# Kernel optimization log

Hardware: AMD Instinct MI355X
Metric: run time of the kernel (lower is better)

## Reference

```python
import jax, jax.numpy as jnp
import numpy as np
from jax import lax
from jax.scipy.linalg import lu_factor, lu_solve

NFEAT = 1024
NHID = 256   # QP variable dimension n
NCLS = 10
NEQ = 64     # equality constraints
QPEN = 0.1   # Qpenalty: Q = QPEN * I
ITERS = 12   # fixed Mehrotra predictor-corrector iterations
BATCH = 128


def setup_inputs() -> dict:
    key = jax.random.key(0)
    ks = jax.random.split(key, 6)
    x = jax.random.normal(ks[0], (BATCH, NFEAT), jnp.float32)
    W1 = jax.random.normal(ks[1], (NHID, NFEAT), jnp.float32) / np.sqrt(NFEAT)
    b1 = jnp.zeros((NHID,), jnp.float32)
    W2 = jax.random.normal(ks[2], (NCLS, NHID), jnp.float32) / np.sqrt(NHID)
    b2 = jnp.zeros((NCLS,), jnp.float32)
    A = jax.random.uniform(ks[3], (NEQ, NHID), jnp.float32)  # torch.rand in module
    return {"x": x, "W1": W1, "b1": b1, "W2": W2, "b2": b2, "A": A}


def _qp_solve(p, A):
    """Batched primal-dual interior-point solve of
        min_z 0.5*QPEN*||z||^2 + p.z   s.t.  A z = b (=1),  z >= 0
    which is the module's QP with Q=QPEN*I, G=-I, h=0, b=1.
    p: (B, n), A: (neq, n). Returns z: (B, n)."""
    B, n = p.shape
    neq = A.shape[0]
    N = n + neq
    b_eq = jnp.ones((neq,), p.dtype)
    rr = jnp.arange(n)

    # warm start: equality-constrained QP (ignore z>=0): [Q A'; A 0][z;nu]=[-p;b]
    K0 = jnp.zeros((N, N), p.dtype)
    K0 = K0.at[rr, rr].set(QPEN)
    K0 = K0.at[:n, n:].set(A.T).at[n:, :n].set(A)
    rhs0 = jnp.concatenate([-p, jnp.broadcast_to(b_eq, (B, neq))], axis=-1)
    sol0 = jnp.linalg.solve(K0, rhs0[..., None])[..., 0]
    z0 = sol0[:, :n]
    nu0 = sol0[:, n:]
    s0 = jnp.maximum(z0, 1.0)          # slack for -z + s = 0, kept positive
    lam0 = jnp.ones((B, n), p.dtype)   # ineq duals

    def step_len(v, dv, w, dw):
        def rat(a, da):
            safe = jnp.where(da < 0, da, -1.0)
            return jnp.where(da < 0, -a / safe, 1e10)
        m = jnp.min(jnp.minimum(rat(v, dv), rat(w, dw)), axis=-1)
        return jnp.minimum(1.0, 0.999 * m)  # (B,)

    def body(carry, _):
        z, s, lam, nu = carry
        rx = QPEN * z + p - lam + nu @ A      # Q z + p + G'lam + A'nu  (G=-I)
        ri = s - z                            # G z + s - h
        re = z @ A.T - b_eq                   # A z - b
        D = lam / s
        Hd = QPEN + D                         # (B, n) diag of Q + G'DG

        # reduced KKT: [[diag(Hd), A'],[A, 0]]  per sample
        K = jnp.zeros((B, N, N), p.dtype)
        K = K.at[:, rr, rr].set(Hd)
        K = K.at[:, :n, n:].set(A.T)
        K = K.at[:, n:, :n].set(A)
        lu, piv = lu_factor(K)

        def solve(rs):
            top = -rx + (lam * ri - rs) / s
            rhs = jnp.concatenate([top, -re], axis=-1)
            sol = lu_solve((lu, piv), rhs[..., None])[..., 0]
            dz = sol[:, :n]
            dnu = sol[:, n:]
            ds = dz - ri                      # ds = -ri - G dz
            dlam = (lam * ri - rs) / s - D * dz
            return dz, ds, dlam, dnu

        # predictor (affine)
        dz_a, ds_a, dlam_a, dnu_a = solve(lam * s)
        a_aff = step_len(s, ds_a, lam, dlam_a)[:, None]
        mu = jnp.mean(s * lam, axis=-1)
        mu_a = jnp.mean((s + a_aff * ds_a) * (lam + a_aff * dlam_a), axis=-1)
        sigma = (mu_a / mu) ** 3
        # corrector
        rs_c = lam * s + ds_a * dlam_a - (sigma * mu)[:, None]
        dz, ds, dlam, dnu = solve(rs_c)
        a = step_len(s, ds, lam, dlam)[:, None]
        z = z + a * dz
        nu = nu + a * dnu
        s = jnp.maximum(s + a * ds, 1e-8)
        lam = jnp.maximum(lam + a * dlam, 1e-8)
        return (z, s, lam, nu), None

    (z, _, _, _), _ = lax.scan(body, (z0, s0, lam0, nu0), None, length=ITERS)
    return z


def reference(x, W1, b1, W2, b2, A):
    h = jax.nn.relu(x @ W1.T + b1)            # fc1 + relu
    z = _qp_solve(-h, A)                      # QPFunction with p = -h
    logits = z @ W2.T + b2                    # fc2
    return jax.nn.log_softmax(logits, axis=-1)
```

## Files before the change

### kernel.cpp

```cpp
#include <hip/hip_runtime.h>
#include <math.h>

#define NTH 512

__device__ __forceinline__ float rl(float v, int ln) {
  return __int_as_float(__builtin_amdgcn_readlane(__float_as_int(v), ln));
}

__device__ __forceinline__ float dot64_row(const float4* __restrict__ As4,
                                           const float4* __restrict__ v4, int t) {
  float acc = 0.f;
#pragma unroll
  for (int q = 0; q < 16; ++q) {
    int qq = (q + t) & 15;
    float4 a = As4[t * 16 + qq];
    float4 b = v4[qq];
    acc = fmaf(a.x, b.x, acc); acc = fmaf(a.y, b.y, acc);
    acc = fmaf(a.z, b.z, acc); acc = fmaf(a.w, b.w, acc);
  }
  return acc;
}

__device__ __forceinline__ void fs_half(const float4* __restrict__ As4,
                                        const float4* __restrict__ wv4,
                                        int bi, int bj, int c0,
                                        float4& o0, float4& o1, float4& o2, float4& o3) {
  float a00=0,a01=0,a02=0,a03=0,a10=0,a11=0,a12=0,a13=0;
  float a20=0,a21=0,a22=0,a23=0,a30=0,a31=0,a32=0,a33=0;
  const int c40 = c0 >> 2;
  for (int c4 = c40; c4 < c40 + 32; ++c4) {
    float4 w4 = wv4[c4];
#pragma unroll
    for (int e = 0; e < 4; ++e) {
      float wc = (e==0)?w4.x:(e==1)?w4.y:(e==2)?w4.z:w4.w;
      int c = 4*c4 + e;
      float4 a4 = As4[c*16 + bi];
      float4 b4 = As4[c*16 + bj];
      float bx = b4.x*wc, by = b4.y*wc, bz = b4.z*wc, bw = b4.w*wc;
      a00=fmaf(a4.x,bx,a00); a01=fmaf(a4.x,by,a01); a02=fmaf(a4.x,bz,a02); a03=fmaf(a4.x,bw,a03);
      a10=fmaf(a4.y,bx,a10); a11=fmaf(a4.y,by,a11); a12=fmaf(a4.y,bz,a12); a13=fmaf(a4.y,bw,a13);
      a20=fmaf(a4.z,bx,a20); a21=fmaf(a4.z,by,a21); a22=fmaf(a4.z,bz,a22); a23=fmaf(a4.z,bw,a23);
      a30=fmaf(a4.w,bx,a30); a31=fmaf(a4.w,by,a31); a32=fmaf(a4.w,bz,a32); a33=fmaf(a4.w,bw,a33);
    }
  }
  o0 = make_float4(a00,a01,a02,a03);
  o1 = make_float4(a10,a11,a12,a13);
  o2 = make_float4(a20,a21,a22,a23);
  o3 = make_float4(a30,a31,a32,a33);
}

#define PSTEP8(VE, V1,V2,V3,V4,V5,V6,V7, LNE) {                        \
    float piv = __shfl(VE, (LNE), 64);                                 \
    float inv = 1.0f / piv;                                            \
    VE = (lane == (LNE)) ? inv : VE * inv;                             \
    float c1 = __shfl(V1,(LNE),64); V1 = (lane==(LNE))?(-c1*inv):fmaf(-c1,VE,V1); \
    float c2 = __shfl(V2,(LNE),64); V2 = (lane==(LNE))?(-c2*inv):fmaf(-c2,VE,V2); \
    float c3 = __shfl(V3,(LNE),64); V3 = (lane==(LNE))?(-c3*inv):fmaf(-c3,VE,V3); \
    float c4_ = __shfl(V4,(LNE),64); V4 = (lane==(LNE))?(-c4_*inv):fmaf(-c4_,VE,V4); \
    float c5 = __shfl(V5,(LNE),64); V5 = (lane==(LNE))?(-c5*inv):fmaf(-c5,VE,V5); \
    float c6 = __shfl(V6,(LNE),64); V6 = (lane==(LNE))?(-c6*inv):fmaf(-c6,VE,V6); \
    float c7 = __shfl(V7,(LNE),64); V7 = (lane==(LNE))?(-c7*inv):fmaf(-c7,VE,V7); \
  }

__device__ __forceinline__ void gj8(float* __restrict__ Sb, float* __restrict__ T,
                                    float* __restrict__ colb, int t) {
  float4* Sb4 = (float4*)Sb;
  float4* T4 = (float4*)T;
  float4* colb4 = (float4*)colb;
  const int lane = t & 63, wav = t >> 6;
  for (int p = 0; p < 8; ++p) {
    if (wav == 0) {
      float v0 = Sb[(8*p+0)*68 + lane];
      float v1 = Sb[(8*p+1)*68 + lane];
      float v2 = Sb[(8*p+2)*68 + lane];
      float v3 = Sb[(8*p+3)*68 + lane];
      float v4 = Sb[(8*p+4)*68 + lane];
      float v5 = Sb[(8*p+5)*68 + lane];
      float v6 = Sb[(8*p+6)*68 + lane];
      float v7 = Sb[(8*p+7)*68 + lane];
      PSTEP8(v0, v1,v2,v3,v4,v5,v6,v7, 8*p+0);
      PSTEP8(v1, v0,v2,v3,v4,v5,v6,v7, 8*p+1);
      PSTEP8(v2, v0,v1,v3,v4,v5,v6,v7, 8*p+2);
      PSTEP8(v3, v0,v1,v2,v4,v5,v6,v7, 8*p+3);
      PSTEP8(v4, v0,v1,v2,v3,v5,v6,v7, 8*p+4);
      PSTEP8(v5, v0,v1,v2,v3,v4,v6,v7, 8*p+5);
      PSTEP8(v6, v0,v1,v2,v3,v4,v5,v7, 8*p+6);
      PSTEP8(v7, v0,v1,v2,v3,v4,v5,v6, 8*p+7);
      T[0*64+lane]=v0; T[1*64+lane]=v1; T[2*64+lane]=v2; T[3*64+lane]=v3;
      T[4*64+lane]=v4; T[5*64+lane]=v5; T[6*64+lane]=v6; T[7*64+lane]=v7;
    } else if (wav == 1) {
      colb4[lane]      = *(const float4*)&Sb[lane*68 + 8*p];
      colb4[64 + lane] = *(const float4*)&Sb[lane*68 + 8*p + 4];
    }
    __syncthreads();
    float4 cA = colb4[lane];
    float4 cB = colb4[64 + lane];
    const bool rowsJ = ((lane >> 3) == p);
    const int e = lane & 7;
#pragma unroll
    for (int q = 0; q < 2; ++q) {
      const int c = 2*wav + q;
      if (rowsJ) {
        Sb4[lane*17 + c] = T4[e*16 + c];
      } else {
        float4 t0=T4[0*16+c], t1=T4[1*16+c], t2=T4[2*16+c], t3=T4[3*16+c];
        float4 t4=T4[4*16+c], t5=T4[5*16+c], t6=T4[6*16+c], t7=T4[7*16+c];
        float4 mv;
        if (c == 2*p || c == 2*p+1) { mv = make_float4(0.f,0.f,0.f,0.f); }
        else mv = Sb4[lane*17 + c];
        mv.x -= cA.x*t0.x + cA.y*t1.x + cA.z*t2.x + cA.w*t3.x
              + cB.x*t4.x + cB.y*t5.x + cB.z*t6.x + cB.w*t7.x;
        mv.y -= cA.x*t0.y + cA.y*t1.y + cA.z*t2.y + cA.w*t3.y
              + cB.x*t4.y + cB.y*t5.y + cB.z*t6.y + cB.w*t7.y;
        mv.z -= cA.x*t0.z + cA.y*t1.z + cA.z*t2.z + cA.w*t3.z
              + cB.x*t4.z + cB.y*t5.z + cB.z*t6.z + cB.w*t7.z;
        mv.w -= cA.x*t0.w + cA.y*t1.w + cA.z*t2.w + cA.w*t3.w
              + cB.x*t4.w + cB.y*t5.w + cB.z*t6.w + cB.w*t7.w;
        Sb4[lane*17 + c] = mv;
      }
    }
    __syncthreads();
  }
}

__device__ __forceinline__ float matS_lds(const float* __restrict__ Sb, float rh, int t) {
  const float4* Sb4 = (const float4*)Sb;
  float acc = 0.f;
#pragma unroll
  for (int m = 0; m < 16; ++m) {
    float4 s4 = Sb4[t*17 + m];
    acc = fmaf(s4.x, rl(rh, 4*m+0), acc);
    acc = fmaf(s4.y, rl(rh, 4*m+1), acc);
    acc = fmaf(s4.z, rl(rh, 4*m+2), acc);
    acc = fmaf(s4.w, rl(rh, 4*m+3), acc);
  }
  return acc;
}

__global__ __launch_bounds__(NTH, 1)
void optnet_kernel(const float* __restrict__ x,  const float* __restrict__ W1,
                   const float* __restrict__ b1, const float* __restrict__ W2,
                   const float* __restrict__ b2, const float* __restrict__ A,
                   float* __restrict__ out)
{
  extern __shared__ float sm[];
  const int b = blockIdx.x;
  const int t = threadIdx.x;
  const int lane = t & 63;
  const int wav = t >> 6;
  const bool owner = (t < 256);

  float* As    = sm;
  float* Sb    = sm + 16384;
  float* xld   = Sb;
  float* Pbuf  = sm + 20736;
  float* T     = Pbuf + 2176;
  float* colb  = T + 512;
  float* h     = colb + 512;
  float* z     = h + 256;
  float* wHd   = z + 256;
  float* wtp   = wHd + 256;
  float* partA = wtp + 256;
  float* partB = partA + 192;
  float* partB2= partB + 192;
  float* nu    = partB2 + 512;
  float* rev   = nu + 64;
  float* dnu   = rev + 64;
  float* red   = dnu + 64;

  const float4* As4  = (const float4*)As;
  float4*       Sb4  = (float4*)Sb;
  const float4* wv4  = (const float4*)wHd;
  const float4* nu4  = (const float4*)nu;
  const float4* dnu4 = (const float4*)dnu;
  float4*       Pb4  = (float4*)Pbuf;

  int bi = 0, bj = 0;
  if (t < 272) {
    int rr = (t < 136) ? t : (t - 136);
    while (rr >= 16 - bi) { rr -= 16 - bi; ++bi; }
    bj = bi + rr;
  }
  const int pg  = (t - 272) >> 6;
  const int plo = pg * 85 + (pg > 0 ? 1 : 0);
  const int phi = plo + 85 + (pg == 0 ? 1 : 0);

  for (int g = t; g < 64 * 256; g += NTH)
    As[(g & 255) * 64 + (g >> 8)] = A[g];
  for (int g = t; g < 1024; g += NTH)
    xld[g] = x[b * 1024 + g];
  __syncthreads();

  {
    const float4* xr = (const float4*)xld;
    for (int jj = 0; jj < 32; ++jj) {
      int j = (wav << 5) + jj;
      const float4* w1r = (const float4*)(W1 + (size_t)j * 1024);
      float acc = 0.f;
#pragma unroll
      for (int mm = 0; mm < 4; ++mm) {
        float4 a = w1r[lane + (mm << 6)];
        float4 xv = xr[lane + (mm << 6)];
        acc = fmaf(a.x,xv.x,fmaf(a.y,xv.y,fmaf(a.z,xv.z,fmaf(a.w,xv.w,acc))));
      }
#pragma unroll
      for (int off = 32; off > 0; off >>= 1) acc += __shfl_xor(acc, off, 64);
      if (lane == 0) { float v = acc + b1[j]; h[j] = v > 0.f ? v : 0.f; }
    }
  }
  __syncthreads();
  const float hr = h[t & 255];

  if (owner) { wHd[t] = 10.0f; wtp[t] = hr * 10.0f; }
  __syncthreads();
  float4 o0, o1, o2, o3;
  if (t < 272) {
    fs_half(As4, wv4, bi, bj, (t < 136) ? 0 : 128, o0, o1, o2, o3);
    if (t >= 136) {
      int tt = t - 136;
      Pb4[tt*4+0]=o0; Pb4[tt*4+1]=o1; Pb4[tt*4+2]=o2; Pb4[tt*4+3]=o3;
    }
  } else if (t < 464) {
    float accB = 0.f;
    for (int c = plo; c < phi; ++c)
      accB = fmaf(wtp[c], As[c * 64 + lane], accB);
    partB[pg * 64 + lane] = accB;
  }
  __syncthreads();
  if (t < 136) {
    float4 p0=Pb4[t*4+0], p1=Pb4[t*4+1], p2=Pb4[t*4+2], p3=Pb4[t*4+3];
    o0.x+=p0.x; o0.y+=p0.y; o0.z+=p0.z; o0.w+=p0.w;
    o1.x+=p1.x; o1.y+=p1.y; o1.z+=p1.z; o1.w+=p1.w;
    o2.x+=p2.x; o2.y+=p2.y; o2.z+=p2.z; o2.w+=p2.w;
    o3.x+=p3.x; o3.y+=p3.y; o3.z+=p3.z; o3.w+=p3.w;
    Sb4[(4*bi+0)*17 + bj] = o0;
    Sb4[(4*bi+1)*17 + bj] = o1;
    Sb4[(4*bi+2)*17 + bj] = o2;
    Sb4[(4*bi+3)*17 + bj] = o3;
    if (bi != bj) {
      Sb4[(4*bj+0)*17 + bi] = make_float4(o0.x,o1.x,o2.x,o3.x);
      Sb4[(4*bj+1)*17 + bi] = make_float4(o0.y,o1.y,o2.y,o3.y);
      Sb4[(4*bj+2)*17 + bi] = make_float4(o0.z,o1.z,o2.z,o3.z);
      Sb4[(4*bj+3)*17 + bi] = make_float4(o0.w,o1.w,o2.w,o3.w);
    }
  }
  __syncthreads();
  gj8(Sb, T, colb, t);
  if (t < 64) {
    float rh = partB[t] + partB[64 + t] + partB[128 + t] - 1.0f;
    nu[t] = matS_lds(Sb, rh, t);
  }
  __syncthreads();

  float zt = 0.f, st = 0.f, lt = 0.f;
  if (owner) {
    float atd = dot64_row(As4, nu4, t);
    zt = (hr - atd) * 10.0f;
    z[t] = zt;
    st = fmaxf(zt, 1.0f);
    lt = 1.0f;
  }
  __syncthreads();

  float rit = 0.f, Dt = 0.f, wt = 0.f, g1 = 0.f, top1 = 0.f, rxt = 0.f;
  for (int it = 0; it < 12; ++it) {
    if (owner) {
      const float nuA = dot64_row(As4, nu4, t);
      rxt = 0.1f * zt - hr - lt + nuA;
      rit = st - zt;
      Dt  = lt / st;
      wt  = 1.0f / (0.1f + Dt);
      const float rs1 = lt * st;
      g1  = (lt * rit - rs1) / st;
      top1 = -rxt + g1;
      wHd[t] = wt;
      wtp[t] = top1 * wt;
    }
    __syncthreads();
    if (t < 272) {
      fs_half(As4, wv4, bi, bj, (t < 136) ? 0 : 128, o0, o1, o2, o3);
      if (t >= 136) {
        int tt = t - 136;
        Pb4[tt*4+0]=o0; Pb4[tt*4+1]=o1; Pb4[tt*4+2]=o2; Pb4[tt*4+3]=o3;
      }
    } else if (t < 464) {
      float accA = 0.f, accB = 0.f;
      for (int c = plo; c < phi; ++c) {
        float av = As[c * 64 + lane];
        accA = fmaf(z[c],   av, accA);
        accB = fmaf(wtp[c], av, accB);
      }
      partA[pg * 64 + lane] = accA;
      partB[pg * 64 + lane] = accB;
    }
    __syncthreads();
    if (t < 136) {
      float4 p0=Pb4[t*4+0], p1=Pb4[t*4+1], p2=Pb4[t*4+2], p3=Pb4[t*4+3];
      o0.x+=p0.x; o0.y+=p0.y; o0.z+=p0.z; o0.w+=p0.w;
      o1.x+=p1.x; o1.y+=p1.y; o1.z+=p1.z; o1.w+=p1.w;
      o2.x+=p2.x; o2.y+=p2.y; o2.z+=p2.z; o2.w+=p2.w;
      o3.x+=p3.x; o3.y+=p3.y; o3.z+=p3.z; o3.w+=p3.w;
      Sb4[(4*bi+0)*17 + bj] = o0;
      Sb4[(4*bi+1)*17 + bj] = o1;
      Sb4[(4*bi+2)*17 + bj] = o2;
      Sb4[(4*bi+3)*17 + bj] = o3;
      if (bi != bj) {
        Sb4[(4*bj+0)*17 + bi] = make_float4(o0.x,o1.x,o2.x,o3.x);
        Sb4[(4*bj+1)*17 + bi] = make_float4(o0.y,o1.y,o2.y,o3.y);
        Sb4[(4*bj+2)*17 + bi] = make_float4(o0.z,o1.z,o2.z,o3.z);
        Sb4[(4*bj+3)*17 + bi] = make_float4(o0.w,o1.w,o2.w,o3.w);
      }
    }
    __syncthreads();
    gj8(Sb, T, colb, t);
    if (t < 64) {
      float re_t = partA[t] + partA[64 + t] + partA[128 + t] - 1.0f;
      rev[t] = re_t;
      float rh = partB[t] + partB[64 + t] + partB[128 + t] + re_t;
      dnu[t] = matS_lds(Sb, rh, t);
    }
    __syncthreads();
    float dsa = 0.f, dla = 0.f;
    if (owner) {
      float atd = dot64_row(As4, dnu4, t);
      float dza = (top1 - atd) * wt;
      dsa = dza - rit;
      dla = g1 - Dt * dza;
      float r1 = dsa < 0.f ? -st / dsa : 1e10f;
      float r2 = dla < 0.f ? -lt / dla : 1e10f;
      float mn = fminf(r1, r2);
#pragma unroll
      for (int off = 32; off > 0; off >>= 1) mn = fminf(mn, __shfl_xor(mn, off, 64));
      if (lane == 0) red[wav] = mn;
    }
    __syncthreads();
    float a_aff = 0.f;
    if (owner) {
      a_aff = fminf(1.0f, 0.999f * fminf(fminf(red[0],red[1]), fminf(red[2],red[3])));
      float p1 = st * lt;
      float p2 = (st + a_aff * dsa) * (lt + a_aff * dla);
#pragma unroll
      for (int off = 32; off > 0; off >>= 1) { p1 += __shfl_xor(p1,off,64); p2 += __shfl_xor(p2,off,64); }
      if (lane == 0) { red[4 + wav] = p1; red[8 + wav] = p2; }
    }
    __syncthreads();
    if (owner) {
      const float mu  = (red[4] + red[5] + red[6]  + red[7])  * (1.0f / 256.0f);
      const float mua = (red[8] + red[9] + red[10] + red[11]) * (1.0f / 256.0f);
      float sig = mua / mu; sig = sig * sig * sig;
      const float smu = sig * mu;
      const float rs2 = lt * st + dsa * dla - smu;
      const float g2  = (lt * rit - rs2) / st;
      const float top2 = -rxt + g2;
      wtp[t] = top2 * wt;
    }
    __syncthreads();
    {
      float accB = 0.f;
      for (int cc = 0; cc < 32; ++cc) {
        int c = (wav << 5) + cc;
        accB = fmaf(wtp[c], As[c * 64 + lane], accB);
      }
      partB2[t] = accB;
    }
    __syncthreads();
    if (t < 64) {
      float rh = partB2[t] + partB2[64+t] + partB2[128+t] + partB2[192+t]
               + partB2[256+t] + partB2[320+t] + partB2[384+t] + partB2[448+t]
               + rev[t];
      dnu[t] = matS_lds(Sb, rh, t);
    }
    __syncthreads();
    float ds2 = 0.f, dl2 = 0.f, dz2 = 0.f;
    if (owner) {
      float atd = dot64_row(As4, dnu4, t);
      const float top2 = wtp[t] / wt;
      dz2 = (top2 - atd) * wt;
      ds2 = dz2 - rit;
      dl2 = (top2 + rxt) - Dt * dz2;
      float r1 = ds2 < 0.f ? -st / ds2 : 1e10f;
      float r2 = dl2 < 0.f ? -lt / dl2 : 1e10f;
      float mn = fminf(r1, r2);
#pragma unroll
      for (int off = 32; off > 0; off >>= 1) mn = fminf(mn, __shfl_xor(mn, off, 64));
      if (lane == 0) red[wav] = mn;
    }
    __syncthreads();
    if (owner) {
      const float a = fminf(1.0f, 0.999f * fminf(fminf(red[0],red[1]), fminf(red[2],red[3])));
      zt += a * dz2;
      st = fmaxf(st + a * ds2, 1e-8f);
      lt = fmaxf(lt + a * dl2, 1e-8f);
      z[t] = zt;
      if (t < 64) nu[t] += a * dnu[t];
    }
    __syncthreads();
  }

  if (t < 160) {
    int cls = t >> 4, pp = t & 15;
    float acc = 0.f;
#pragma unroll
    for (int e = 0; e < 16; ++e) {
      int c = (pp << 4) + e;
      acc = fmaf(z[c], W2[cls * 256 + c], acc);
    }
    partA[t] = acc;
  }
  __syncthreads();
  if (t < 10) {
    float s = b2[t];
#pragma unroll
    for (int pp = 0; pp < 16; ++pp) s += partA[(t << 4) + pp];
    red[t] = s;
  }
  __syncthreads();
  if (t == 0) {
    float mx = red[0];
#pragma unroll
    for (int c = 1; c < 10; ++c) mx = fmaxf(mx, red[c]);
    float se = 0.f;
#pragma unroll
    for (int c = 0; c < 10; ++c) se += expf(red[c] - mx);
    float lse = mx + logf(se);
    for (int c = 0; c < 10; ++c) out[b * 10 + c] = red[c] - lse;
  }
}

extern "C" void kernel_launch(void* const* d_in, const int* in_sizes, int n_in,
                              void* d_out, int out_size, void* d_ws, size_t ws_size,
                              hipStream_t stream) {
  (void)in_sizes; (void)n_in; (void)out_size; (void)d_ws; (void)ws_size;
  const float* x  = (const float*)d_in[0];
  const float* W1 = (const float*)d_in[1];
  const float* b1 = (const float*)d_in[2];
  const float* W2 = (const float*)d_in[3];
  const float* b2 = (const float*)d_in[4];
  const float* A  = (const float*)d_in[5];
  float* out = (float*)d_out;

  const size_t shmem = (16384 + 4352 + 2176 + 512 + 512 + 4*256 + 192 + 192 + 512 + 3*64 + 16)
                       * sizeof(float);
  (void)hipFuncSetAttribute((const void*)optnet_kernel,
                            hipFuncAttributeMaxDynamicSharedMemorySize, (int)shmem);
  optnet_kernel<<<128, NTH, shmem, stream>>>(x, W1, b1, W2, b2, A, out);
}
```

Baseline: 504.3 us.

## Pipeline Gauss-Jordan pivot blocks across waves and merge step-length reductions

Rewrites the 64x64 Gauss-Jordan inversion so each wave owns an 8-row block, updates it in place, and the next pivot wave factors its block right after its update. This removes the separate T/colb staging buffers and one barrier per pivot block. It also expands mu_aff as a quadratic in the step length, so the three sums are reduced in one pass and a block-wide barrier and reduction round is dropped. The risks are a different floating-point summation order and a reliance on each wave writing back only its own rows within a step.

```diff
diff --git a/kernel.cpp b/kernel.cpp
--- a/kernel.cpp
+++ b/kernel.cpp
@@ -62,62 +62,64 @@
     float c7 = __shfl(V7,(LNE),64); V7 = (lane==(LNE))?(-c7*inv):fmaf(-c7,VE,V7); \
   }
 
-__device__ __forceinline__ void gj8(float* __restrict__ Sb, float* __restrict__ T,
-                                    float* __restrict__ colb, int t) {
-  float4* Sb4 = (float4*)Sb;
-  float4* T4 = (float4*)T;
-  float4* colb4 = (float4*)colb;
+__device__ __forceinline__ void gj8p(float* __restrict__ Sb, int t) {
   const int lane = t & 63, wav = t >> 6;
+  if (wav == 0) {
+    float v0 = Sb[0*68+lane], v1 = Sb[1*68+lane], v2 = Sb[2*68+lane], v3 = Sb[3*68+lane];
+    float v4 = Sb[4*68+lane], v5 = Sb[5*68+lane], v6 = Sb[6*68+lane], v7 = Sb[7*68+lane];
+    PSTEP8(v0, v1,v2,v3,v4,v5,v6,v7, 0);
+    PSTEP8(v1, v0,v2,v3,v4,v5,v6,v7, 1);
+    PSTEP8(v2, v0,v1,v3,v4,v5,v6,v7, 2);
+    PSTEP8(v3, v0,v1,v2,v4,v5,v6,v7, 3);
+    PSTEP8(v4, v0,v1,v2,v3,v5,v6,v7, 4);
+    PSTEP8(v5, v0,v1,v2,v3,v4,v6,v7, 5);
+    PSTEP8(v6, v0,v1,v2,v3,v4,v5,v7, 6);
+    PSTEP8(v7, v0,v1,v2,v3,v4,v5,v6, 7);
+    Sb[0*68+lane]=v0; Sb[1*68+lane]=v1; Sb[2*68+lane]=v2; Sb[3*68+lane]=v3;
+    Sb[4*68+lane]=v4; Sb[5*68+lane]=v5; Sb[6*68+lane]=v6; Sb[7*68+lane]=v7;
+  }
+  __syncthreads();
   for (int p = 0; p < 8; ++p) {
-    if (wav == 0) {
-      float v0 = Sb[(8*p+0)*68 + lane];
-      float v1 = Sb[(8*p+1)*68 + lane];
-      float v2 = Sb[(8*p+2)*68 + lane];
-      float v3 = Sb[(8*p+3)*68 + lane];
-      float v4 = Sb[(8*p+4)*68 + lane];
-      float v5 = Sb[(8*p+5)*68 + lane];
-      float v6 = Sb[(8*p+6)*68 + lane];
-      float v7 = Sb[(8*p+7)*68 + lane];
-      PSTEP8(v0, v1,v2,v3,v4,v5,v6,v7, 8*p+0);
-      PSTEP8(v1, v0,v2,v3,v4,v5,v6,v7, 8*p+1);
-      PSTEP8(v2, v0,v1,v3,v4,v5,v6,v7, 8*p+2);
-      PSTEP8(v3, v0,v1,v2,v4,v5,v6,v7, 8*p+3);
-      PSTEP8(v4, v0,v1,v2,v3,v5,v6,v7, 8*p+4);
-      PSTEP8(v5, v0,v1,v2,v3,v4,v6,v7, 8*p+5);
-      PSTEP8(v6, v0,v1,v2,v3,v4,v5,v7, 8*p+6);
-      PSTEP8(v7, v0,v1,v2,v3,v4,v5,v6, 8*p+7);
-      T[0*64+lane]=v0; T[1*64+lane]=v1; T[2*64+lane]=v2; T[3*64+lane]=v3;
-      T[4*64+lane]=v4; T[5*64+lane]=v5; T[6*64+lane]=v6; T[7*64+lane]=v7;
-    } else if (wav == 1) {
-      colb4[lane]      = *(const float4*)&Sb[lane*68 + 8*p];
-      colb4[64 + lane] = *(const float4*)&Sb[lane*68 + 8*p + 4];
-    }
-    __syncthreads();
-    float4 cA = colb4[lane];
-    float4 cB = colb4[64 + lane];
-    const bool rowsJ = ((lane >> 3) == p);
-    const int e = lane & 7;
-#pragma unroll
-    for (int q = 0; q < 2; ++q) {
-      const int c = 2*wav + q;
-      if (rowsJ) {
-        Sb4[lane*17 + c] = T4[e*16 + c];
-      } else {
-        float4 t0=T4[0*16+c], t1=T4[1*16+c], t2=T4[2*16+c], t3=T4[3*16+c];
-        float4 t4=T4[4*16+c], t5=T4[5*16+c], t6=T4[6*16+c], t7=T4[7*16+c];
-        float4 mv;
-        if (c == 2*p || c == 2*p+1) { mv = make_float4(0.f,0.f,0.f,0.f); }
-        else mv = Sb4[lane*17 + c];
-        mv.x -= cA.x*t0.x + cA.y*t1.x + cA.z*t2.x + cA.w*t3.x
-              + cB.x*t4.x + cB.y*t5.x + cB.z*t6.x + cB.w*t7.x;
-        mv.y -= cA.x*t0.y + cA.y*t1.y + cA.z*t2.y + cA.w*t3.y
-              + cB.x*t4.y + cB.y*t5.y + cB.z*t6.y + cB.w*t7.y;
-        mv.z -= cA.x*t0.z + cA.y*t1.z + cA.z*t2.z + cA.w*t3.z
-              + cB.x*t4.z + cB.y*t5.z + cB.z*t6.z + cB.w*t7.z;
-        mv.w -= cA.x*t0.w + cA.y*t1.w + cA.z*t2.w + cA.w*t3.w
-              + cB.x*t4.w + cB.y*t5.w + cB.z*t6.w + cB.w*t7.w;
-        Sb4[lane*17 + c] = mv;
-      }
+    if (wav != p) {
+      const int prow = 8 * p;
+      const int r0 = 8 * wav;
+      float t0 = Sb[(prow+0)*68+lane], t1 = Sb[(prow+1)*68+lane];
+      float t2 = Sb[(prow+2)*68+lane], t3 = Sb[(prow+3)*68+lane];
+      float t4 = Sb[(prow+4)*68+lane], t5 = Sb[(prow+5)*68+lane];
+      float t6 = Sb[(prow+6)*68+lane], t7 = Sb[(prow+7)*68+lane];
+      const bool pivc = (lane >= prow) && (lane < prow + 8);
+      float m0 = pivc ? 0.f : Sb[(r0+0)*68+lane];
+      float m1 = pivc ? 0.f : Sb[(r0+1)*68+lane];
+      float m2 = pivc ? 0.f : Sb[(r0+2)*68+lane];
+      float m3 = pivc ? 0.f : Sb[(r0+3)*68+lane];
+      float m4 = pivc ? 0.f : Sb[(r0+4)*68+lane];
+      float m5 = pivc ? 0.f : Sb[(r0+5)*68+lane];
+      float m6 = pivc ? 0.f : Sb[(r0+6)*68+lane];
+      float m7 = pivc ? 0.f : Sb[(r0+7)*68+lane];
+#define GJUPD(MR, RR) {                                                    \
+        const float4* cp = (const float4*)&Sb[(r0+(RR))*68 + prow];        \
+        float4 cA = cp[0], cB = cp[1];                                     \
+        MR -= cA.x*t0 + cA.y*t1 + cA.z*t2 + cA.w*t3                        \
+            + cB.x*t4 + cB.y*t5 + cB.z*t6 + cB.w*t7;                       \
+      }
+      GJUPD(m0,0) GJUPD(m1,1) GJUPD(m2,2) GJUPD(m3,3)
+      GJUPD(m4,4) GJUPD(m5,5) GJUPD(m6,6) GJUPD(m7,7)
+#undef GJUPD
+      if (p < 7 && wav == p + 1) {
+        const int pb = 8 * (p + 1);
+        PSTEP8(m0, m1,m2,m3,m4,m5,m6,m7, pb+0);
+        PSTEP8(m1, m0,m2,m3,m4,m5,m6,m7, pb+1);
+        PSTEP8(m2, m0,m1,m3,m4,m5,m6,m7, pb+2);
+        PSTEP8(m3, m0,m1,m2,m4,m5,m6,m7, pb+3);
+        PSTEP8(m4, m0,m1,m2,m3,m5,m6,m7, pb+4);
+        PSTEP8(m5, m0,m1,m2,m3,m4,m6,m7, pb+5);
+        PSTEP8(m6, m0,m1,m2,m3,m4,m5,m7, pb+6);
+        PSTEP8(m7, m0,m1,m2,m3,m4,m5,m6, pb+7);
+      }
+      Sb[(r0+0)*68+lane]=m0; Sb[(r0+1)*68+lane]=m1;
+      Sb[(r0+2)*68+lane]=m2; Sb[(r0+3)*68+lane]=m3;
+      Sb[(r0+4)*68+lane]=m4; Sb[(r0+5)*68+lane]=m5;
+      Sb[(r0+6)*68+lane]=m6; Sb[(r0+7)*68+lane]=m7;
     }
     __syncthreads();
   }
@@ -154,9 +156,7 @@
   float* Sb    = sm + 16384;
   float* xld   = Sb;
   float* Pbuf  = sm + 20736;
-  float* T     = Pbuf + 2176;
-  float* colb  = T + 512;
-  float* h     = colb + 512;
+  float* h     = Pbuf + 2176;
   float* z     = h + 256;
   float* wHd   = z + 256;
   float* wtp   = wHd + 256;
@@ -245,7 +245,7 @@
     }
   }
   __syncthreads();
-  gj8(Sb, T, colb, t);
+  gj8p(Sb, t);
   if (t < 64) {
     float rh = partB[t] + partB[64 + t] + partB[128 + t] - 1.0f;
     nu[t] = matS_lds(Sb, rh, t);
@@ -312,7 +312,7 @@
       }
     }
     __syncthreads();
-    gj8(Sb, T, colb, t);
+    gj8p(Sb, t);
     if (t < 64) {
       float re_t = partA[t] + partA[64 + t] + partA[128 + t] - 1.0f;
       rev[t] = re_t;
@@ -329,24 +329,28 @@
       float r1 = dsa < 0.f ? -st / dsa : 1e10f;
       float r2 = dla < 0.f ? -lt / dla : 1e10f;
       float mn = fminf(r1, r2);
-#pragma unroll
-      for (int off = 32; off > 0; off >>= 1) mn = fminf(mn, __shfl_xor(mn, off, 64));
-      if (lane == 0) red[wav] = mn;
-    }
-    __syncthreads();
-    float a_aff = 0.f;
+      float q0 = st * lt;
+      float q1 = st * dla + dsa * lt;
+      float q2 = dsa * dla;
+#pragma unroll
+      for (int off = 32; off > 0; off >>= 1) {
+        mn = fminf(mn, __shfl_xor(mn, off, 64));
+        q0 += __shfl_xor(q0, off, 64);
+        q1 += __shfl_xor(q1, off, 64);
+        q2 += __shfl_xor(q2, off, 64);
+      }
+      if (lane == 0) {
+        red[wav] = mn; red[4+wav] = q0; red[8+wav] = q1; red[12+wav] = q2;
+      }
+    }
+    __syncthreads();
     if (owner) {
-      a_aff = fminf(1.0f, 0.999f * fminf(fminf(red[0],red[1]), fminf(red[2],red[3])));
-      float p1 = st * lt;
-      float p2 = (st + a_aff * dsa) * (lt + a_aff * dla);
-#pragma unroll
-      for (int off = 32; off > 0; off >>= 1) { p1 += __shfl_xor(p1,off,64); p2 += __shfl_xor(p2,off,64); }
-      if (lane == 0) { red[4 + wav] = p1; red[8 + wav] = p2; }
-    }
-    __syncthreads();
-    if (owner) {
-      const float mu  = (red[4] + red[5] + red[6]  + red[7])  * (1.0f / 256.0f);
-      const float mua = (red[8] + red[9] + red[10] + red[11]) * (1.0f / 256.0f);
+      const float a_aff = fminf(1.0f, 0.999f * fminf(fminf(red[0],red[1]), fminf(red[2],red[3])));
+      const float S0 = red[4] + red[5] + red[6] + red[7];
+      const float S1 = red[8] + red[9] + red[10] + red[11];
+      const float S2 = red[12] + red[13] + red[14] + red[15];
+      const float mu  = S0 * (1.0f / 256.0f);
+      const float mua = (S0 + a_aff * S1 + a_aff * a_aff * S2) * (1.0f / 256.0f);
       float sig = mua / mu; sig = sig * sig * sig;
       const float smu = sig * mu;
       const float rs2 = lt * st + dsa * dla - smu;
@@ -439,7 +443,7 @@
   const float* A  = (const float*)d_in[5];
   float* out = (float*)d_out;
 
-  const size_t shmem = (16384 + 4352 + 2176 + 512 + 512 + 4*256 + 192 + 192 + 512 + 3*64 + 16)
+  const size_t shmem = (16384 + 4352 + 2176 + 4*256 + 192 + 192 + 512 + 3*64 + 16)
                        * sizeof(float);
   (void)hipFuncSetAttribute((const void*)optnet_kernel,
                             hipFuncAttributeMaxDynamicSharedMemorySize, (int)shmem);
```

Measured after the change: 587.1 us. 16.4% more time.

## Merge IPM per-iteration prologue into update step and fuse mu reductions

Applied to the files above, without the earlier changes.

The per-iteration residual setup now runs inside the previous iteration's update block, and nu·A is tracked incrementally (nuA += a*A·dnu) instead of recomputed with a 64-wide dot. That removes one barrier and one dot product per iteration. The affine mu is expanded as a quadratic in the step length (S0 + a*S1 + a^2*S2), so all sums reduce in a single pass with the step-length min, removing another barrier. The incremental nu update and the algebraic rewrite change floating-point rounding slightly, and nu itself is no longer updated.

```diff
diff --git a/kernel.cpp b/kernel.cpp
--- a/kernel.cpp
+++ b/kernel.cpp
@@ -252,31 +252,26 @@
   }
   __syncthreads();
 
-  float zt = 0.f, st = 0.f, lt = 0.f;
+  float zt = 0.f, st = 0.f, lt = 0.f, nuA = 0.f;
+  float rxt = 0.f, rit = 0.f, Dt = 0.f, wt = 0.f, g1 = 0.f, top1 = 0.f;
   if (owner) {
-    float atd = dot64_row(As4, nu4, t);
-    zt = (hr - atd) * 10.0f;
+    nuA = dot64_row(As4, nu4, t);
+    zt = (hr - nuA) * 10.0f;
     z[t] = zt;
     st = fmaxf(zt, 1.0f);
     lt = 1.0f;
-  }
-  __syncthreads();
-
-  float rit = 0.f, Dt = 0.f, wt = 0.f, g1 = 0.f, top1 = 0.f, rxt = 0.f;
+    rxt = 0.1f * zt - hr - lt + nuA;
+    rit = st - zt;
+    Dt  = lt / st;
+    wt  = 1.0f / (0.1f + Dt);
+    g1  = -Dt * zt;
+    top1 = -rxt + g1;
+    wHd[t] = wt;
+    wtp[t] = top1 * wt;
+  }
+  __syncthreads();
+
   for (int it = 0; it < 12; ++it) {
-    if (owner) {
-      const float nuA = dot64_row(As4, nu4, t);
-      rxt = 0.1f * zt - hr - lt + nuA;
-      rit = st - zt;
-      Dt  = lt / st;
-      wt  = 1.0f / (0.1f + Dt);
-      const float rs1 = lt * st;
-      g1  = (lt * rit - rs1) / st;
-      top1 = -rxt + g1;
-      wHd[t] = wt;
-      wtp[t] = top1 * wt;
-    }
-    __syncthreads();
     if (t < 272) {
       fs_half(As4, wv4, bi, bj, (t < 136) ? 0 : 128, o0, o1, o2, o3);
       if (t >= 136) {
@@ -329,29 +324,33 @@
       float r1 = dsa < 0.f ? -st / dsa : 1e10f;
       float r2 = dla < 0.f ? -lt / dla : 1e10f;
       float mn = fminf(r1, r2);
-#pragma unroll
-      for (int off = 32; off > 0; off >>= 1) mn = fminf(mn, __shfl_xor(mn, off, 64));
-      if (lane == 0) red[wav] = mn;
-    }
-    __syncthreads();
-    float a_aff = 0.f;
+      float q0 = st * lt;
+      float q1 = st * dla + dsa * lt;
+      float q2 = dsa * dla;
+#pragma unroll
+      for (int off = 32; off > 0; off >>= 1) {
+        mn = fminf(mn, __shfl_xor(mn, off, 64));
+        q0 += __shfl_xor(q0, off, 64);
+        q1 += __shfl_xor(q1, off, 64);
+        q2 += __shfl_xor(q2, off, 64);
+      }
+      if (lane == 0) {
+        red[wav] = mn; red[4+wav] = q0; red[8+wav] = q1; red[12+wav] = q2;
+      }
+    }
+    __syncthreads();
+    float top2 = 0.f;
     if (owner) {
-      a_aff = fminf(1.0f, 0.999f * fminf(fminf(red[0],red[1]), fminf(red[2],red[3])));
-      float p1 = st * lt;
-      float p2 = (st + a_aff * dsa) * (lt + a_aff * dla);
-#pragma unroll
-      for (int off = 32; off > 0; off >>= 1) { p1 += __shfl_xor(p1,off,64); p2 += __shfl_xor(p2,off,64); }
-      if (lane == 0) { red[4 + wav] = p1; red[8 + wav] = p2; }
-    }
-    __syncthreads();
-    if (owner) {
-      const float mu  = (red[4] + red[5] + red[6]  + red[7])  * (1.0f / 256.0f);
-      const float mua = (red[8] + red[9] + red[10] + red[11]) * (1.0f / 256.0f);
+      const float a_aff = fminf(1.0f, 0.999f * fminf(fminf(red[0],red[1]), fminf(red[2],red[3])));
+      const float S0 = red[4] + red[5] + red[6] + red[7];
+      const float S1 = red[8] + red[9] + red[10] + red[11];
+      const float S2 = red[12] + red[13] + red[14] + red[15];
+      const float mu  = S0 * (1.0f / 256.0f);
+      const float mua = (S0 + a_aff * S1 + a_aff * a_aff * S2) * (1.0f / 256.0f);
       float sig = mua / mu; sig = sig * sig * sig;
       const float smu = sig * mu;
-      const float rs2 = lt * st + dsa * dla - smu;
-      const float g2  = (lt * rit - rs2) / st;
-      const float top2 = -rxt + g2;
+      const float g2  = g1 + (smu - dsa * dla) / st;
+      top2 = -rxt + g2;
       wtp[t] = top2 * wt;
     }
     __syncthreads();
@@ -371,11 +370,10 @@
       dnu[t] = matS_lds(Sb, rh, t);
     }
     __syncthreads();
-    float ds2 = 0.f, dl2 = 0.f, dz2 = 0.f;
+    float ds2 = 0.f, dl2 = 0.f, dz2 = 0.f, atd2 = 0.f;
     if (owner) {
-      float atd = dot64_row(As4, dnu4, t);
-      const float top2 = wtp[t] / wt;
-      dz2 = (top2 - atd) * wt;
+      atd2 = dot64_row(As4, dnu4, t);
+      dz2 = (top2 - atd2) * wt;
       ds2 = dz2 - rit;
       dl2 = (top2 + rxt) - Dt * dz2;
       float r1 = ds2 < 0.f ? -st / ds2 : 1e10f;
@@ -392,7 +390,15 @@
       st = fmaxf(st + a * ds2, 1e-8f);
       lt = fmaxf(lt + a * dl2, 1e-8f);
       z[t] = zt;
-      if (t < 64) nu[t] += a * dnu[t];
+      nuA = fmaf(a, atd2, nuA);
+      rxt = 0.1f * zt - hr - lt + nuA;
+      rit = st - zt;
+      Dt  = lt / st;
+      wt  = 1.0f / (0.1f + Dt);
+      g1  = -Dt * zt;
+      top1 = -rxt + g1;
+      wHd[t] = wt;
+      wtp[t] = top1 * wt;
     }
     __syncthreads();
   }
```

Measured after the change: 485.3 us. -3.8%, faster.
